# Performance work log

Hardware: AMD Instinct MI355X
Metric: run time of the kernel (lower is better)

## Reference

```python
import jax, jax.numpy as jnp
import numpy as np

S, H, A = 16384, 1024, 1024


def setup_inputs() -> dict:
    key = jax.random.key(0)
    k1, k2, k3, k4, k5, k6 = jax.random.split(key, 6)
    enc_out = jax.random.normal(k1, (S, 1, H), dtype=jnp.float32)
    dec_h = jax.random.normal(k2, (1, H), dtype=jnp.float32)
    mask = jax.random.randint(k3, (S, 1), 0, 2) == 1  # bool [S,1]
    # learned params (torch Linear stores weight as [out, in]; y = x @ W.T)
    W2_dec = jax.random.normal(k4, (A, H), dtype=jnp.float32) * 0.02
    W1_enc = jax.random.normal(k5, (A, H), dtype=jnp.float32) * 0.02
    V = jax.random.normal(k6, (1, A), dtype=jnp.float32) * 0.02
    return {"enc_out": enc_out, "dec_h": dec_h, "mask": mask,
            "W2_dec": W2_dec, "W1_enc": W1_enc, "V": V}


def reference(enc_out, dec_h, mask, W2_dec, W1_enc, V):
    enc = jnp.squeeze(enc_out, axis=1)            # [S, H]
    d = dec_h @ W2_dec.T                          # [1, A]
    e = enc @ W1_enc.T                            # [S, A]
    u = jnp.tanh(d + e) @ V.T                     # [S, 1]
    u = jnp.where(mask, -jnp.inf, u)              # masked logits (returned, like in-place fill)
    a = jax.nn.softmax(u, axis=0)                 # softmax over seq dim
    out = jnp.sum(a * enc, axis=0)                # [H]
    return (out, u)
```

## Files before the change

kernel.cpp:

```cpp
#include <hip/hip_runtime.h>
#include <math.h>
#include <stdint.h>

#define S_DIM 16384
#define H_DIM 1024
#define A_DIM 1024

#define MASK_NEG (-3.0e38f)

typedef __attribute__((ext_vector_type(8))) _Float16 f16x8;
typedef __attribute__((ext_vector_type(4))) float f32x4;
typedef __attribute__((address_space(3))) uint32_t as3_u32;
typedef __attribute__((address_space(1))) uint32_t as1_u32;

__device__ __forceinline__ float fast_tanh(float x) {
    float e = __expf(2.0f * x);
    return 1.0f - 2.0f * __builtin_amdgcn_rcpf(e + 1.0f);
}


__global__ __launch_bounds__(256) void prep_kernel(
        const float* __restrict__ enc, _Float16* __restrict__ enc_h,
        const float* __restrict__ W1, _Float16* __restrict__ W1_h,
        const float* __restrict__ dec_h, const float* __restrict__ W2,
        float* __restrict__ d, float* __restrict__ u_acc) {
    const int b = blockIdx.x;
    const int t = threadIdx.x;
    if (b < 8704) {
        const float* src = (b < 8192) ? enc : W1;
        _Float16* dst    = (b < 8192) ? enc_h : W1_h;
        const int i = ((b < 8192) ? b : (b - 8192)) * 256 + t;
        float4 v0 = ((const float4*)src)[2 * i];
        float4 v1 = ((const float4*)src)[2 * i + 1];
        union { _Float16 h[8]; uint4 u; } pk;
        pk.h[0] = (_Float16)v0.x; pk.h[1] = (_Float16)v0.y;
        pk.h[2] = (_Float16)v0.z; pk.h[3] = (_Float16)v0.w;
        pk.h[4] = (_Float16)v1.x; pk.h[5] = (_Float16)v1.y;
        pk.h[6] = (_Float16)v1.z; pk.h[7] = (_Float16)v1.w;
        const int s  = i >> 7;
        const int g  = i & 127;
        const int kt = g >> 2;
        const int cg = g & 3;
        const int r  = s & 255;
        const int tb = s >> 8;
        const int slot = (cg - (r >> 1)) & 3;
        ((uint4*)dst)[(size_t)(tb * 16 + kt) * 1024 + r * 4 + slot] = pk.u;
        if (b < 64) u_acc[b * 256 + t] = 0.0f;
    } else {
        const int a = b - 8704;
        const float* row = W2 + (size_t)a * H_DIM;
        float s = 0.0f;
        for (int h = t; h < H_DIM; h += 256) s += dec_h[h] * row[h];
        #pragma unroll
        for (int off = 32; off; off >>= 1) s += __shfl_down(s, off, 64);
        __shared__ float wsum[4];
        if ((t & 63) == 0) wsum[t >> 6] = s;
        __syncthreads();
        if (t == 0) d[a] = wsum[0] + wsum[1] + wsum[2] + wsum[3];
    }
}

__global__ __launch_bounds__(512, 1) void fused_gemm_f16_2ph(
        const _Float16* __restrict__ Ag,
        const _Float16* __restrict__ Bg,
        const float* __restrict__ V,
        const float* __restrict__ d,
        float* __restrict__ u_acc) {
    __shared__ __align__(16) _Float16 AB[2][32768];

    const int tid  = threadIdx.x;
    const int wave = tid >> 6;
    const int lane = tid & 63;
    const int quad = lane >> 4;
    const int l16  = lane & 15;
    const int wm   = wave >> 2;
    const int wn   = wave & 3;
    const int s0   = blockIdx.x * 256;
    const int a0   = blockIdx.y * 256;

    const int rowoff = (wave & 3) * 64;
    const _Float16* gtile = ((wave < 4)
            ? Ag + (size_t)blockIdx.x * (16 * 8192)
            : Bg + (size_t)blockIdx.y * (16 * 8192))
          + rowoff * 32 + lane * 8;
    _Float16* lbase0 = &AB[0][((wave < 4) ? 0 : 8192) + rowoff * 32];

    const int sw = ((quad - (l16 >> 1)) & 3) * 8;
    int aoff[8], boff[4];
    #pragma unroll
    for (int mi = 0; mi < 8; ++mi)
        aoff[mi] = (wm * 128 + mi * 16 + l16) * 32 + sw;
    #pragma unroll
    for (int ni = 0; ni < 4; ++ni)
        boff[ni] = 8192 + (wn * 64 + ni * 16 + l16) * 32 + sw;

    f32x4 acc[8][4];
    #pragma unroll
    for (int mi = 0; mi < 8; ++mi)
        #pragma unroll
        for (int ni = 0; ni < 4; ++ni)
            acc[mi][ni] = (f32x4){0.f, 0.f, 0.f, 0.f};

    const _Float16* hAB = &AB[0][0];

    #pragma unroll
    for (int s = 0; s < 2; ++s)
        #pragma unroll
        for (int j = 0; j < 4; ++j)
            __builtin_amdgcn_global_load_lds(
                (const as1_u32*)(const void*)(gtile + s * 8192 + j * 512),
                (as3_u32*)(void*)(lbase0 + s * 16384 + j * 512), 16, 0, 0);

    for (int ph = 0; ph < 16; ++ph) {
        const int b = ph & 1;
        if (ph < 15) {
            #pragma unroll
            for (int s = 0; s < 2; ++s)
                #pragma unroll
                for (int j = 0; j < 4; ++j)
                    __builtin_amdgcn_global_load_lds(
                        (const as1_u32*)(const void*)(gtile + ((ph + 1) * 2 + s) * 8192 + j * 512),
                        (as3_u32*)(void*)(lbase0 + (b ^ 1) * 32768 + s * 16384 + j * 512),
                        16, 0, 0);
            asm volatile("s_waitcnt vmcnt(8)" ::: "memory");
        } else {
            asm volatile("s_waitcnt vmcnt(0)" ::: "memory");
        }
        __builtin_amdgcn_sched_barrier(0);
        __builtin_amdgcn_s_barrier();
        __builtin_amdgcn_sched_barrier(0);

        __builtin_amdgcn_s_setprio(1);
        #pragma unroll
        for (int s = 0; s < 2; ++s) {
            const int base = b * 32768 + s * 16384;
            f16x8 bf[4];
            #pragma unroll
            for (int ni = 0; ni < 4; ++ni)
                bf[ni] = *(const f16x8*)&hAB[base + boff[ni]];
            #pragma unroll
            for (int mi = 0; mi < 8; ++mi) {
                f16x8 af = *(const f16x8*)&hAB[base + aoff[mi]];
                #pragma unroll
                for (int ni = 0; ni < 4; ++ni)
                    acc[mi][ni] = __builtin_amdgcn_mfma_f32_16x16x32_f16(af, bf[ni], acc[mi][ni], 0, 0, 0);
            }
        }
        __builtin_amdgcn_s_setprio(0);
        __builtin_amdgcn_sched_barrier(0);

        if (ph < 15) {
            __builtin_amdgcn_s_barrier();
            __builtin_amdgcn_sched_barrier(0);
        }
    }

    float* P = (float*)&AB[0][0];
    float vv[4], dd[4];
    #pragma unroll
    for (int ni = 0; ni < 4; ++ni) {
        int c = a0 + wn * 64 + ni * 16 + l16;
        vv[ni] = V[c];
        dd[ni] = d[c];
    }
    #pragma unroll
    for (int mi = 0; mi < 8; ++mi) {
        #pragma unroll
        for (int reg = 0; reg < 4; ++reg) {
            float s = 0.0f;
            #pragma unroll
            for (int ni = 0; ni < 4; ++ni)
                s += vv[ni] * fast_tanh(dd[ni] + acc[mi][ni][reg]);
            #pragma unroll
            for (int off = 1; off < 16; off <<= 1)
                s += __shfl_xor(s, off, 64);
            if (l16 == 0)
                P[(wm * 128 + mi * 16 + quad * 4 + reg) * 4 + wn] = s;
        }
    }
    __syncthreads();
    if (tid < 256)
        atomicAdd(u_acc + s0 + tid,
                  P[tid * 4 + 0] + P[tid * 4 + 1] + P[tid * 4 + 2] + P[tid * 4 + 3]);
}

__global__ __launch_bounds__(512, 2) void fused_gemm_f16(
        const _Float16* __restrict__ Ag, const _Float16* __restrict__ Bg,
        const float* __restrict__ V, const float* __restrict__ d,
        float* __restrict__ u_acc) {
    __shared__ __align__(16) _Float16 AB[2][16384];

    const int tid  = threadIdx.x;
    const int wave = tid >> 6;
    const int lane = tid & 63;
    const int quad = lane >> 4;
    const int l16  = lane & 15;
    const int wm   = wave >> 2;
    const int wn   = wave & 3;
    const int s0   = blockIdx.x * 256;
    const int a0   = blockIdx.y * 256;

    const int rowoff = (wave & 3) * 64;
    const _Float16* gtile = ((wave < 4)
            ? Ag + (size_t)blockIdx.x * (16 * 8192)
            : Bg + (size_t)blockIdx.y * (16 * 8192))
          + rowoff * 32 + lane * 8;
    _Float16* lbase0 = &AB[0][((wave < 4) ? 0 : 8192) + rowoff * 32];

    const int sw = ((quad - (l16 >> 1)) & 3) * 8;
    int aoff[8], boff[4];
    #pragma unroll
    for (int mi = 0; mi < 8; ++mi)
        aoff[mi] = (wm * 128 + mi * 16 + l16) * 32 + sw;
    #pragma unroll
    for (int ni = 0; ni < 4; ++ni)
        boff[ni] = 8192 + (wn * 64 + ni * 16 + l16) * 32 + sw;

    f32x4 acc[8][4];
    #pragma unroll
    for (int mi = 0; mi < 8; ++mi)
        #pragma unroll
        for (int ni = 0; ni < 4; ++ni)
            acc[mi][ni] = (f32x4){0.f, 0.f, 0.f, 0.f};

    #pragma unroll
    for (int j = 0; j < 4; ++j)
        __builtin_amdgcn_global_load_lds(
            (const as1_u32*)(const void*)(gtile + j * 512),
            (as3_u32*)(void*)(lbase0 + j * 512), 16, 0, 0);
    __syncthreads();

    for (int kt = 0; kt < H_DIM / 32; kt += 2) {
        {
            #pragma unroll
            for (int j = 0; j < 4; ++j)
                __builtin_amdgcn_global_load_lds(
                    (const as1_u32*)(const void*)(gtile + (kt + 1) * 8192 + j * 512),
                    (as3_u32*)(void*)(lbase0 + 16384 + j * 512), 16, 0, 0);
        }
        {
            f16x8 bf[4];
            #pragma unroll
            for (int ni = 0; ni < 4; ++ni) bf[ni] = *(const f16x8*)&AB[0][boff[ni]];
            #pragma unroll
            for (int mi = 0; mi < 8; ++mi) {
                f16x8 af = *(const f16x8*)&AB[0][aoff[mi]];
                #pragma unroll
                for (int ni = 0; ni < 4; ++ni)
                    acc[mi][ni] = __builtin_amdgcn_mfma_f32_16x16x32_f16(af, bf[ni], acc[mi][ni], 0, 0, 0);
            }
        }
        __syncthreads();
        if (kt + 2 < H_DIM / 32) {
            #pragma unroll
            for (int j = 0; j < 4; ++j)
                __builtin_amdgcn_global_load_lds(
                    (const as1_u32*)(const void*)(gtile + (kt + 2) * 8192 + j * 512),
                    (as3_u32*)(void*)(lbase0 + j * 512), 16, 0, 0);
        }
        {
            f16x8 bf[4];
            #pragma unroll
            for (int ni = 0; ni < 4; ++ni) bf[ni] = *(const f16x8*)&AB[1][boff[ni]];
            #pragma unroll
            for (int mi = 0; mi < 8; ++mi) {
                f16x8 af = *(const f16x8*)&AB[1][aoff[mi]];
                #pragma unroll
                for (int ni = 0; ni < 4; ++ni)
                    acc[mi][ni] = __builtin_amdgcn_mfma_f32_16x16x32_f16(af, bf[ni], acc[mi][ni], 0, 0, 0);
            }
        }
        __syncthreads();
    }

    float* P = (float*)&AB[0][0];
    float vv[4], dd[4];
    #pragma unroll
    for (int ni = 0; ni < 4; ++ni) {
        int c = a0 + wn * 64 + ni * 16 + l16;
        vv[ni] = V[c];
        dd[ni] = d[c];
    }
    #pragma unroll
    for (int mi = 0; mi < 8; ++mi) {
        #pragma unroll
        for (int reg = 0; reg < 4; ++reg) {
            float s = 0.0f;
            #pragma unroll
            for (int ni = 0; ni < 4; ++ni)
                s += vv[ni] * fast_tanh(dd[ni] + acc[mi][ni][reg]);
            #pragma unroll
            for (int off = 1; off < 16; off <<= 1)
                s += __shfl_xor(s, off, 64);
            if (l16 == 0)
                P[(wm * 128 + mi * 16 + quad * 4 + reg) * 4 + wn] = s;
        }
    }
    __syncthreads();
    if (tid < 256)
        atomicAdd(u_acc + s0 + tid,
                  P[tid * 4 + 0] + P[tid * 4 + 1] + P[tid * 4 + 2] + P[tid * 4 + 3]);
}

__global__ __launch_bounds__(256) void fused_gemm(const float* __restrict__ enc,
                                                  const float* __restrict__ W1,
                                                  const float* __restrict__ V,
                                                  const float* __restrict__ d,
                                                  float* __restrict__ u_acc) {
    __shared__ __align__(16) float As[16][128 + 4];
    __shared__ __align__(16) float Bs[16][128 + 4];
    const int tid = threadIdx.x;
    const int tx = tid & 15, ty = tid >> 4;
    const int s0 = blockIdx.y * 128, a0 = blockIdx.x * 128;
    const int lr = tid >> 2, lc = tid & 3;
    float acc[8][8] = {};
    for (int kt = 0; kt < H_DIM / 16; ++kt) {
        const int k0 = kt * 16;
        float4 av0 = *(const float4*)(enc + (size_t)(s0 + lr)      * H_DIM + k0 + 4 * lc);
        float4 av1 = *(const float4*)(enc + (size_t)(s0 + lr + 64) * H_DIM + k0 + 4 * lc);
        float4 bv0 = *(const float4*)(W1  + (size_t)(a0 + lr)      * H_DIM + k0 + 4 * lc);
        float4 bv1 = *(const float4*)(W1  + (size_t)(a0 + lr + 64) * H_DIM + k0 + 4 * lc);
        __syncthreads();
        As[4*lc+0][lr] = av0.x; As[4*lc+1][lr] = av0.y; As[4*lc+2][lr] = av0.z; As[4*lc+3][lr] = av0.w;
        As[4*lc+0][lr+64] = av1.x; As[4*lc+1][lr+64] = av1.y; As[4*lc+2][lr+64] = av1.z; As[4*lc+3][lr+64] = av1.w;
        Bs[4*lc+0][lr] = bv0.x; Bs[4*lc+1][lr] = bv0.y; Bs[4*lc+2][lr] = bv0.z; Bs[4*lc+3][lr] = bv0.w;
        Bs[4*lc+0][lr+64] = bv1.x; Bs[4*lc+1][lr+64] = bv1.y; Bs[4*lc+2][lr+64] = bv1.z; Bs[4*lc+3][lr+64] = bv1.w;
        __syncthreads();
        #pragma unroll
        for (int k = 0; k < 16; ++k) {
            float4 A0 = *(const float4*)&As[k][8 * ty];
            float4 A1 = *(const float4*)&As[k][8 * ty + 4];
            float4 B0 = *(const float4*)&Bs[k][8 * tx];
            float4 B1 = *(const float4*)&Bs[k][8 * tx + 4];
            float ar[8] = {A0.x, A0.y, A0.z, A0.w, A1.x, A1.y, A1.z, A1.w};
            float br[8] = {B0.x, B0.y, B0.z, B0.w, B1.x, B1.y, B1.z, B1.w};
            #pragma unroll
            for (int i = 0; i < 8; ++i)
                #pragma unroll
                for (int j = 0; j < 8; ++j)
                    acc[i][j] = fmaf(ar[i], br[j], acc[i][j]);
        }
    }
    float vv[8], dd[8];
    #pragma unroll
    for (int j = 0; j < 8; ++j) { int c = a0 + 8 * tx + j; vv[j] = V[c]; dd[j] = d[c]; }
    float pu[8];
    #pragma unroll
    for (int i = 0; i < 8; ++i) {
        float s = 0.0f;
        #pragma unroll
        for (int j = 0; j < 8; ++j) s += vv[j] * fast_tanh(dd[j] + acc[i][j]);
        pu[i] = s;
    }
    __syncthreads();
    float* Pf = &As[0][0];
    #pragma unroll
    for (int i = 0; i < 8; ++i) Pf[(8 * ty + i) * 16 + tx] = pu[i];
    __syncthreads();
    if (tid < 128) {
        float s = 0.0f;
        #pragma unroll
        for (int j = 0; j < 16; ++j) s += Pf[tid * 16 + j];
        atomicAdd(u_acc + s0 + tid, s);
    }
}

__global__ __launch_bounds__(1024) void softmax_kernel(const float* __restrict__ u_acc,
                                                       const void* __restrict__ mask,
                                                       float* __restrict__ u_out,
                                                       float* __restrict__ p) {
    const int t = threadIdx.x;
    const unsigned char* mb = (const unsigned char*)mask;
    const int* mi = (const int*)mask;

    unsigned int orv = 0;
    for (int i = t; i < S_DIM; i += 1024)
        if (i & 3) orv |= mb[i];
    __shared__ int sflag;
    if (t == 0) sflag = 0;
    __syncthreads();
    if (orv) sflag = 1;
    __syncthreads();
    const int bytemask = sflag;

    float v[16];
    float lmax = -INFINITY;
    #pragma unroll
    for (int i = 0; i < 16; ++i) {
        int r = t + i * 1024;
        int m = bytemask ? (int)mb[r] : mi[r];
        float val = m ? MASK_NEG : u_acc[r];
        u_out[r] = val;
        v[i] = val;
        lmax = fmaxf(lmax, val);
    }

    __shared__ float red[16];
    __shared__ float sm, sdenom;
    #pragma unroll
    for (int off = 32; off; off >>= 1) lmax = fmaxf(lmax, __shfl_down(lmax, off, 64));
    int wid = t >> 6, lane = t & 63;
    if (lane == 0) red[wid] = lmax;
    __syncthreads();
    if (t == 0) {
        float m2 = -INFINITY;
        for (int i = 0; i < 16; ++i) m2 = fmaxf(m2, red[i]);
        sm = m2;
    }
    __syncthreads();
    const float m = sm;

    float lsum = 0.0f;
    #pragma unroll
    for (int i = 0; i < 16; ++i) {
        v[i] = expf(v[i] - m);
        lsum += v[i];
    }
    #pragma unroll
    for (int off = 32; off; off >>= 1) lsum += __shfl_down(lsum, off, 64);
    if (lane == 0) red[wid] = lsum;
    __syncthreads();
    if (t == 0) {
        float s2 = 0.0f;
        for (int i = 0; i < 16; ++i) s2 += red[i];
        sdenom = s2;
    }
    __syncthreads();
    const float inv = 1.0f / sdenom;
    #pragma unroll
    for (int i = 0; i < 16; ++i) p[t + i * 1024] = v[i] * inv;
}

__global__ __launch_bounds__(256) void wsum_part(const _Float16* __restrict__ enc_h,
                                                 const float* __restrict__ p,
                                                 float* __restrict__ part) {
    const int t = threadIdx.x;
    const int b = blockIdx.x;
    const int kt    = t >> 3;
    const int cg    = (t >> 1) & 3;
    const int inner = (t & 1) * 4;
    float4 acc = {0.f, 0.f, 0.f, 0.f};
    const int s0 = b * 32;
    for (int s = s0; s < s0 + 32; ++s) {
        float ps = p[s];
        const int r  = s & 255;
        const int tb = s >> 8;
        const int slot = (cg - (r >> 1)) & 3;
        size_t off = ((size_t)(tb * 16 + kt) << 13) + (r << 5) + slot * 8 + inner;
        union { _Float16 h[4]; uint2 u; } e;
        e.u = *(const uint2*)(enc_h + off);
        acc.x += ps * (float)e.h[0];
        acc.y += ps * (float)e.h[1];
        acc.z += ps * (float)e.h[2];
        acc.w += ps * (float)e.h[3];
    }
    ((float4*)(part + (size_t)b * 1024))[t] = acc;
}
__global__ __launch_bounds__(256) void wsum_reduce(const float* __restrict__ part,
                                                   float* __restrict__ out) {
    __shared__ float red[256];
    const int t = threadIdx.x;
    const int col = blockIdx.x * 16 + (t & 15);
    const int seg = t >> 4;
    float s = 0.0f;
    for (int b = seg * 32; b < seg * 32 + 32; ++b)
        s += part[(size_t)b * 1024 + col];
    red[t] = s;
    __syncthreads();
    if (t < 16) {
        float r = 0.0f;
        #pragma unroll
        for (int k = 0; k < 16; ++k) r += red[k * 16 + t];
        out[col] = r;
    }
}
__global__ __launch_bounds__(256) void weighted_sum(const float* __restrict__ enc,
                                                    const float* __restrict__ p,
                                                    float* __restrict__ out) {
    const int t = threadIdx.x;
    const int s0 = blockIdx.x * 32;
    const float4* encv = (const float4*)enc;
    float4 acc = {0.0f, 0.0f, 0.0f, 0.0f};
    for (int s = s0; s < s0 + 32; ++s) {
        float ps = p[s];
        float4 e = encv[(size_t)s * 256 + t];
        acc.x += ps * e.x; acc.y += ps * e.y; acc.z += ps * e.z; acc.w += ps * e.w;
    }
    atomicAdd(out + 4 * t + 0, acc.x);
    atomicAdd(out + 4 * t + 1, acc.y);
    atomicAdd(out + 4 * t + 2, acc.z);
    atomicAdd(out + 4 * t + 3, acc.w);
}
__global__ void zero_kernel(float* __restrict__ u_acc, float* __restrict__ out) {
    int i = blockIdx.x * 256 + threadIdx.x;
    if (i < S_DIM) u_acc[i] = 0.0f;
    if (i < H_DIM) out[i]   = 0.0f;
}
__global__ __launch_bounds__(256) void dec_proj(const float* __restrict__ dec_h,
                                                const float* __restrict__ W2,
                                                float* __restrict__ d) {
    int a = blockIdx.x;
    int t = threadIdx.x;
    const float* row = W2 + (size_t)a * H_DIM;
    float s = 0.0f;
    for (int h = t; h < H_DIM; h += 256) s += dec_h[h] * row[h];
    #pragma unroll
    for (int off = 32; off; off >>= 1) s += __shfl_down(s, off, 64);
    __shared__ float wsum[4];
    if ((t & 63) == 0) wsum[t >> 6] = s;
    __syncthreads();
    if (t == 0) d[a] = wsum[0] + wsum[1] + wsum[2] + wsum[3];
}

extern "C" void kernel_launch(void* const* d_in, const int* in_sizes, int n_in,
                              void* d_out, int out_size, void* d_ws, size_t ws_size,
                              hipStream_t stream) {
    const float* enc   = (const float*)d_in[0];
    const float* dec_h = (const float*)d_in[1];
    const void*  mask  = d_in[2];
    const float* W2    = (const float*)d_in[3];
    const float* W1    = (const float*)d_in[4];
    const float* V     = (const float*)d_in[5];

    float* out   = (float*)d_out;
    float* u_out = (float*)d_out + H_DIM;

    float* ws    = (float*)d_ws;
    float* d     = ws;
    float* u_acc = ws + A_DIM;
    float* p     = ws + A_DIM + S_DIM;
    float* part  = ws + A_DIM + 2 * S_DIM;
    size_t f_end = (size_t)(A_DIM + 2 * S_DIM + 512 * 1024);
    _Float16* enc_h = (_Float16*)(ws + f_end);
    _Float16* W1_h  = enc_h + (size_t)S_DIM * H_DIM;
    size_t need_bytes = f_end * 4
                      + (size_t)S_DIM * H_DIM * 2
                      + (size_t)A_DIM * H_DIM * 2;

    int dev = 0;
    hipGetDevice(&dev);
    int max_lds = 0;
    hipDeviceGetAttribute(&max_lds, hipDeviceAttributeMaxSharedMemoryPerBlock, dev);

    if (ws_size >= need_bytes) {
        prep_kernel<<<9728, 256, 0, stream>>>(enc, enc_h, W1, W1_h,
                                              dec_h, W2, d, u_acc);
        if (max_lds >= 131072) {
            fused_gemm_f16_2ph<<<dim3(S_DIM / 256, A_DIM / 256), 512, 0, stream>>>(
                enc_h, W1_h, V, d, u_acc);
        } else {
            fused_gemm_f16<<<dim3(S_DIM / 256, A_DIM / 256), 512, 0, stream>>>(
                enc_h, W1_h, V, d, u_acc);
        }
        softmax_kernel<<<1, 1024, 0, stream>>>(u_acc, mask, u_out, p);
        wsum_part<<<S_DIM / 32, 256, 0, stream>>>(enc_h, p, part);
        wsum_reduce<<<64, 256, 0, stream>>>(part, out);
    } else {
        zero_kernel<<<64, 256, 0, stream>>>(u_acc, out);
        dec_proj<<<A_DIM, 256, 0, stream>>>(dec_h, W2, d);
        fused_gemm<<<dim3(A_DIM / 128, S_DIM / 128), 256, 0, stream>>>(enc, W1, V, d, u_acc);
        softmax_kernel<<<1, 1024, 0, stream>>>(u_acc, mask, u_out, p);
        weighted_sum<<<S_DIM / 32, 256, 0, stream>>>(enc, p, out);
    }
}
```

Baseline: 173.5 us.

## Fuse softmax into weighted-sum via per-block online softmax partials

Removes the single-block softmax kernel. Each weighted-sum block now applies the mask, computes a local max and exp-sum over its 32 rows, and writes them as partials. The reduce kernel rescales those partials to a global max and normalises. Masked rows are skipped in the enc_h loads, and a mask-format detection flag is added to the prep kernel. This removes a serial 1-block launch at the cost of extra reduction work and exp calls in the tail kernels.

```diff
diff --git a/kernel.cpp b/kernel.cpp
--- a/kernel.cpp
+++ b/kernel.cpp
@@ -23,7 +23,8 @@
         const float* __restrict__ enc, _Float16* __restrict__ enc_h,
         const float* __restrict__ W1, _Float16* __restrict__ W1_h,
         const float* __restrict__ dec_h, const float* __restrict__ W2,
-        float* __restrict__ d, float* __restrict__ u_acc) {
+        float* __restrict__ d, float* __restrict__ u_acc,
+        const void* __restrict__ mask, int* __restrict__ mflag) {
     const int b = blockIdx.x;
     const int t = threadIdx.x;
     if (b < 8704) {
@@ -46,7 +47,7 @@
         const int slot = (cg - (r >> 1)) & 3;
         ((uint4*)dst)[(size_t)(tb * 16 + kt) * 1024 + r * 4 + slot] = pk.u;
         if (b < 64) u_acc[b * 256 + t] = 0.0f;
-    } else {
+    } else if (b < 9728) {
         const int a = b - 8704;
         const float* row = W2 + (size_t)a * H_DIM;
         float s = 0.0f;
@@ -57,6 +58,17 @@
         if ((t & 63) == 0) wsum[t >> 6] = s;
         __syncthreads();
         if (t == 0) d[a] = wsum[0] + wsum[1] + wsum[2] + wsum[3];
+    } else {
+        const unsigned char* mb = (const unsigned char*)mask;
+        unsigned int orv = 0;
+        for (int i = t; i < S_DIM; i += 256)
+            if (i & 3) orv |= mb[i];
+        __shared__ int oflag;
+        if (t == 0) oflag = 0;
+        __syncthreads();
+        if (orv) oflag = 1;
+        __syncthreads();
+        if (t == 0) mflag[0] = oflag;
     }
 }
 
@@ -431,49 +443,109 @@
     for (int i = 0; i < 16; ++i) p[t + i * 1024] = v[i] * inv;
 }
 
-__global__ __launch_bounds__(256) void wsum_part(const _Float16* __restrict__ enc_h,
-                                                 const float* __restrict__ p,
-                                                 float* __restrict__ part) {
+__global__ __launch_bounds__(256) void tail_part(
+        const _Float16* __restrict__ enc_h,
+        const float* __restrict__ u_acc,
+        const void* __restrict__ mask,
+        const int* __restrict__ mflag,
+        float* __restrict__ u_out,
+        float* __restrict__ part,
+        float* __restrict__ pm,
+        float* __restrict__ pd) {
     const int t = threadIdx.x;
     const int b = blockIdx.x;
+    const int s0 = b * 32;
+    __shared__ float wsh[32];
+
+    if (t < 32) {
+        const int s = s0 + t;
+        int msk = mflag[0] ? (int)((const unsigned char*)mask)[s]
+                           : ((const int*)mask)[s];
+        float val = msk ? MASK_NEG : u_acc[s];
+        u_out[s] = val;
+        float m_b = val;
+        #pragma unroll
+        for (int off = 16; off; off >>= 1)
+            m_b = fmaxf(m_b, __shfl_xor(m_b, off, 64));
+        float w = msk ? 0.0f : expf(val - m_b);
+        wsh[t] = w;
+        float D = w;
+        #pragma unroll
+        for (int off = 16; off; off >>= 1)
+            D += __shfl_xor(D, off, 64);
+        if (t == 0) { pm[b] = m_b; pd[b] = D; }
+    }
+    __syncthreads();
+
     const int kt    = t >> 3;
     const int cg    = (t >> 1) & 3;
     const int inner = (t & 1) * 4;
     float4 acc = {0.f, 0.f, 0.f, 0.f};
-    const int s0 = b * 32;
-    for (int s = s0; s < s0 + 32; ++s) {
-        float ps = p[s];
-        const int r  = s & 255;
-        const int tb = s >> 8;
-        const int slot = (cg - (r >> 1)) & 3;
-        size_t off = ((size_t)(tb * 16 + kt) << 13) + (r << 5) + slot * 8 + inner;
-        union { _Float16 h[4]; uint2 u; } e;
-        e.u = *(const uint2*)(enc_h + off);
-        acc.x += ps * (float)e.h[0];
-        acc.y += ps * (float)e.h[1];
-        acc.z += ps * (float)e.h[2];
-        acc.w += ps * (float)e.h[3];
+    for (int i = 0; i < 32; ++i) {
+        float w = wsh[i];
+        if (w != 0.0f) {
+            const int s  = s0 + i;
+            const int r  = s & 255;
+            const int tb = s >> 8;
+            const int slot = (cg - (r >> 1)) & 3;
+            size_t off = ((size_t)(tb * 16 + kt) << 13) + (r << 5) + slot * 8 + inner;
+            union { _Float16 h[4]; uint2 u; } e;
+            e.u = *(const uint2*)(enc_h + off);
+            acc.x += w * (float)e.h[0];
+            acc.y += w * (float)e.h[1];
+            acc.z += w * (float)e.h[2];
+            acc.w += w * (float)e.h[3];
+        }
     }
     ((float4*)(part + (size_t)b * 1024))[t] = acc;
 }
-__global__ __launch_bounds__(256) void wsum_reduce(const float* __restrict__ part,
-                                                   float* __restrict__ out) {
+
+__global__ __launch_bounds__(256) void tail_reduce(
+        const float* __restrict__ part, const float* __restrict__ pm,
+        const float* __restrict__ pd, float* __restrict__ out) {
+    __shared__ float scale[512];
     __shared__ float red[256];
+    __shared__ float ginv;
     const int t = threadIdx.x;
+
+    red[t] = fmaxf(pm[t], pm[t + 256]);
+    __syncthreads();
+    #pragma unroll
+    for (int off = 128; off; off >>= 1) {
+        if (t < off) red[t] = fmaxf(red[t], red[t + off]);
+        __syncthreads();
+    }
+    const float gm = red[0];
+    __syncthreads();
+
+    float sc0 = expf(pm[t] - gm);
+    float sc1 = expf(pm[t + 256] - gm);
+    scale[t] = sc0; scale[t + 256] = sc1;
+    red[t] = sc0 * pd[t] + sc1 * pd[t + 256];
+    __syncthreads();
+    #pragma unroll
+    for (int off = 128; off; off >>= 1) {
+        if (t < off) red[t] += red[t + off];
+        __syncthreads();
+    }
+    if (t == 0) ginv = 1.0f / red[0];
+    __syncthreads();
+
     const int col = blockIdx.x * 16 + (t & 15);
     const int seg = t >> 4;
     float s = 0.0f;
-    for (int b = seg * 32; b < seg * 32 + 32; ++b)
-        s += part[(size_t)b * 1024 + col];
+    for (int b2 = seg * 32; b2 < seg * 32 + 32; ++b2)
+        s += scale[b2] * part[(size_t)b2 * 1024 + col];
     red[t] = s;
     __syncthreads();
     if (t < 16) {
         float r = 0.0f;
         #pragma unroll
         for (int k = 0; k < 16; ++k) r += red[k * 16 + t];
-        out[col] = r;
-    }
-}
+        out[col] = r * ginv;
+    }
+}
+
 __global__ __launch_bounds__(256) void weighted_sum(const float* __restrict__ enc,
                                                     const float* __restrict__ p,
                                                     float* __restrict__ out) {
@@ -529,6 +601,9 @@
     float* d     = ws;
     float* u_acc = ws + A_DIM;
     float* p     = ws + A_DIM + S_DIM;
+    float* pm    = p;
+    float* pd    = p + 512;
+    int*   mflag = (int*)(p + 1024);
     float* part  = ws + A_DIM + 2 * S_DIM;
     size_t f_end = (size_t)(A_DIM + 2 * S_DIM + 512 * 1024);
     _Float16* enc_h = (_Float16*)(ws + f_end);
@@ -543,8 +618,8 @@
     hipDeviceGetAttribute(&max_lds, hipDeviceAttributeMaxSharedMemoryPerBlock, dev);
 
     if (ws_size >= need_bytes) {
-        prep_kernel<<<9728, 256, 0, stream>>>(enc, enc_h, W1, W1_h,
-                                              dec_h, W2, d, u_acc);
+        prep_kernel<<<9729, 256, 0, stream>>>(enc, enc_h, W1, W1_h,
+                                              dec_h, W2, d, u_acc, mask, mflag);
         if (max_lds >= 131072) {
             fused_gemm_f16_2ph<<<dim3(S_DIM / 256, A_DIM / 256), 512, 0, stream>>>(
                 enc_h, W1_h, V, d, u_acc);
@@ -552,9 +627,9 @@
             fused_gemm_f16<<<dim3(S_DIM / 256, A_DIM / 256), 512, 0, stream>>>(
                 enc_h, W1_h, V, d, u_acc);
         }
-        softmax_kernel<<<1, 1024, 0, stream>>>(u_acc, mask, u_out, p);
-        wsum_part<<<S_DIM / 32, 256, 0, stream>>>(enc_h, p, part);
-        wsum_reduce<<<64, 256, 0, stream>>>(part, out);
+        tail_part<<<S_DIM / 32, 256, 0, stream>>>(enc_h, u_acc, mask, mflag,
+                                                  u_out, part, pm, pd);
+        tail_reduce<<<64, 256, 0, stream>>>(part, pm, pd, out);
     } else {
         zero_kernel<<<64, 256, 0, stream>>>(u_acc, out);
         dec_proj<<<A_DIM, 256, 0, stream>>>(dec_h, W2, d);
```

After: 181.9 us. +4.8%, slower.
